# Optimization experiments

Measured on AMD Instinct MI355X. Metric: run time of the kernel, lower is better.

## Reference

```python
import jax, jax.numpy as jnp
import numpy as np

HIDDEN = 768
HEADS = 12
HEAD_DIM = 64
SEQ = 512
DS_K = 64  # downsampling_k
EPS = 1e-6


def setup_inputs() -> dict:
    key = jax.random.key(0)
    ks = jax.random.split(key, 16)
    B = 32
    sd = 1.0 / DS_K
    glorot = jax.nn.initializers.lecun_normal()  # flax default_kernel_init
    inp = {
        "query": jax.random.normal(ks[0], (B, SEQ, HIDDEN), jnp.float32),
        "key": jax.random.normal(ks[1], (B, SEQ, HIDDEN), jnp.float32),
        "value": jax.random.normal(ks[2], (B, SEQ, HIDDEN), jnp.float32),
        "step": 0,
        # learned Linformer-style downsampling projections [k, s]
        "W_kds": sd * jax.random.normal(ks[3], (DS_K, SEQ), jnp.float32),
        "W_vds": sd * jax.random.normal(ks[4], (DS_K, SEQ), jnp.float32),
        # DenseGeneral qkv kernels [d, n, h] and biases [n, h]
        "Wq": glorot(ks[5], (HIDDEN, HEADS, HEAD_DIM), jnp.float32),
        "bq": jnp.zeros((HEADS, HEAD_DIM), jnp.float32),
        "Wk": glorot(ks[6], (HIDDEN, HEADS, HEAD_DIM), jnp.float32),
        "bk": jnp.zeros((HEADS, HEAD_DIM), jnp.float32),
        "Wv": glorot(ks[7], (HIDDEN, HEADS, HEAD_DIM), jnp.float32),
        "bv": jnp.zeros((HEADS, HEAD_DIM), jnp.float32),
        # out projection contracts (n, h) -> hidden
        "Wout": glorot(ks[8], (HEADS * HEAD_DIM, HIDDEN), jnp.float32).reshape(HEADS, HEAD_DIM, HIDDEN),
        "bout": jnp.zeros((HIDDEN,), jnp.float32),
    }
    return inp


def reference(query, key, value, step, W_kds, W_vds, Wq, bq, Wk, bk, Wv, bv, Wout, bout):
    # Linformer-style downsample of keys/values along sequence: [b,s,d] -> [b,k,d]
    key_ds = jnp.einsum("ks,bsd->bkd", W_kds, key)
    val_ds = jnp.einsum("ks,bsd->bkd", W_vds, value)

    # per-head projections
    queries = jnp.einsum("bqd,dnh->bqnh", query, Wq) + bq    # [b,q,n,h]
    keys = jnp.einsum("bkd,dnh->bknh", key_ds, Wk) + bk      # [b,k,n,h]
    values = jnp.einsum("bkd,dnh->bknh", val_ds, Wv) + bv    # [b,k,n,h]

    # kernelized linear attention with elu feature map (mask=False path)
    phi_q = jax.nn.elu(queries) + 1.0
    phi_k = jax.nn.elu(keys) + 1.0
    s = jnp.einsum("bknd,bknh->bndh", phi_k, values)          # [b,n,h,h] KV state
    z = jnp.sum(phi_k, axis=1)                                 # [b,n,h]
    qs = jnp.einsum("bqnd,bndh->bqnh", phi_q, s)
    qz = jnp.einsum("bqnd,bnd->bqn", phi_q, z) + EPS
    a_v = qs / qz[..., None]                                   # [b,q,n,h]

    out = jnp.einsum("bqnh,nhD->bqD", a_v, Wout) + bout        # [b,q,hidden]
    return out
```

## Files before the change

### kernel.cpp

```cpp
#include <hip/hip_runtime.h>

typedef unsigned short u16;
typedef u16 u16x4 __attribute__((ext_vector_type(4)));
typedef u16 u16x8 __attribute__((ext_vector_type(8)));
typedef __bf16 bf16;
typedef bf16 bf16x8 __attribute__((ext_vector_type(8)));
typedef float f32x4 __attribute__((ext_vector_type(4)));

__device__ __forceinline__ float bf2f(u16 v) {
  union { unsigned u; float f; } x; x.u = ((unsigned)v) << 16; return x.f;
}
__device__ __forceinline__ u16 f2bf(float f) {
  union { float f; unsigned u; } x; x.f = f;
  unsigned u = x.u;
  u += 0x7fffu + ((u >> 16) & 1u);
  return (u16)(u >> 16);
}
__device__ __forceinline__ unsigned cvt2bf(float lo, float hi) {
  unsigned r;
  asm("v_cvt_pk_bf16_f32 %0, %1, %2" : "=v"(r) : "v"(lo), "v"(hi));
  return r;
}

#define GLDS16(g, l) __builtin_amdgcn_global_load_lds( \
    (const __attribute__((address_space(1))) unsigned int*)(const void*)(g), \
    (__attribute__((address_space(3))) unsigned int*)(void*)(l), 16, 0, 0)

__global__ __launch_bounds__(256) void prep_k(
    const float* __restrict__ Wq, const float* __restrict__ Wk,
    const float* __restrict__ Wv, const float* __restrict__ Wout,
    const float* __restrict__ wkds, const float* __restrict__ wvds,
    const float* __restrict__ b0, const float* __restrict__ b1,
    const float* __restrict__ b2, const float* __restrict__ b3,
    u16* __restrict__ WT, u16* __restrict__ dstW, u16* __restrict__ dstB)
{
  __shared__ u16 T[64][72];
  const int blk = blockIdx.x;
  const int t = threadIdx.x;
  if (blk < 576) {
    const int bz = blk / 144, rr = blk % 144;
    const int r0 = (rr / 12) * 64, c0 = (rr % 12) * 64;
    const float* W = (bz == 0) ? Wq : (bz == 1) ? Wk : (bz == 2) ? Wv : Wout;
    u16* O = WT + (size_t)bz * 768 * 768;
    #pragma unroll
    for (int p = 0; p < 2; ++p) {
      int v = t + p * 256;
      int r = v / 8, c = (v % 8) * 8;
      f32x4 x0 = *(const f32x4*)&W[(size_t)(r0 + r) * 768 + c0 + c];
      f32x4 x1 = *(const f32x4*)&W[(size_t)(r0 + r) * 768 + c0 + c + 4];
      #pragma unroll
      for (int i = 0; i < 4; ++i) { T[r][c + i] = f2bf(x0[i]); T[r][c + 4 + i] = f2bf(x1[i]); }
    }
    __syncthreads();
    #pragma unroll
    for (int p = 0; p < 2; ++p) {
      int v = t + p * 256;
      int r = v / 8, c = (v % 8) * 8;
      u16x8 tv;
      #pragma unroll
      for (int i = 0; i < 8; ++i) tv[i] = T[c + i][r];
      *(u16x8*)&O[(size_t)(c0 + r) * 768 + r0 + c] = tv;
    }
  } else if (blk < 832) {
    const int i = (blk - 576) * 256 + t;
    if (i < 32768) dstW[i] = f2bf(wkds[i]);
    else           dstW[i] = f2bf(wvds[i - 32768]);
  } else {
    const int i = (blk - 832) * 256 + t;
    if (i < 3072) {
      int s = i / 768, si = i % 768;
      const float* src = (s == 0) ? b0 : (s == 1) ? b1 : (s == 2) ? b2 : b3;
      dstB[i] = f2bf(src[si]);
    }
  }
}

__global__ __launch_bounds__(256) void ds_k(
    const u16* __restrict__ Wds,
    const float* __restrict__ key, const float* __restrict__ value,
    u16* __restrict__ key_ds)
{
  __shared__ u16 Bs[2][64 * 40];
  const int pair = blockIdx.y >> 5, b = blockIdx.y & 31;
  const float* src = (pair ? value : key) + (size_t)b * 512 * 768;
  const u16* W = Wds + pair * 32768;
  u16* dst = key_ds + (size_t)pair * 1572864 + (size_t)b * 49152;
  const int nt = blockIdx.x * 64;
  const int t = threadIdx.x, wave = t >> 6, lane = t & 63;
  const int wm = (wave >> 1) * 32, wn = (wave & 1) * 32;
  const int lrow = lane & 15, quad = lane >> 4;
  const int bn = t & 63, bk8 = (t >> 6) * 8;
  const float* bcol = src + nt + bn;

  f32x4 acc[2][2] = {};
  float breg[8];
  bf16x8 av[2][2];

  #pragma unroll
  for (int i = 0; i < 8; ++i) breg[i] = bcol[(size_t)(bk8 + i) * 768];
  #pragma unroll
  for (int i = 0; i < 2; ++i)
    av[0][i] = *(const bf16x8*)&W[(size_t)(wm + i * 16 + lrow) * 512 + quad * 8];

  #pragma unroll
  for (int step = 0; step < 16; ++step) {
    const int cur = step & 1, nxt = cur ^ 1;
    u16x8 wv;
    #pragma unroll
    for (int i = 0; i < 8; ++i) wv[i] = f2bf(breg[i]);
    *(u16x8*)&Bs[cur][bn * 40 + bk8] = wv;
    if (step < 15) {
      const int k1 = (step + 1) * 32;
      #pragma unroll
      for (int i = 0; i < 8; ++i) breg[i] = bcol[(size_t)(k1 + bk8 + i) * 768];
      #pragma unroll
      for (int i = 0; i < 2; ++i)
        av[nxt][i] = *(const bf16x8*)&W[(size_t)(wm + i * 16 + lrow) * 512 + k1 + quad * 8];
    }
    __syncthreads();
    bf16x8 bv[2];
    #pragma unroll
    for (int j = 0; j < 2; ++j)
      bv[j] = *(const bf16x8*)&Bs[cur][(wn + j * 16 + lrow) * 40 + quad * 8];
    #pragma unroll
    for (int i = 0; i < 2; ++i)
      #pragma unroll
      for (int j = 0; j < 2; ++j)
        acc[i][j] = __builtin_amdgcn_mfma_f32_16x16x32_bf16(av[cur][i], bv[j], acc[i][j], 0, 0, 0);
  }

  #pragma unroll
  for (int i = 0; i < 2; ++i)
    #pragma unroll
    for (int j = 0; j < 2; ++j) {
      const int col = nt + wn + j * 16 + lrow;
      #pragma unroll
      for (int r = 0; r < 4; ++r) {
        const int row = wm + i * 16 + quad * 4 + r;
        dst[(size_t)row * 768 + col] = f2bf(acc[i][j][r]);
      }
    }
}

__global__ __launch_bounds__(256) void gemmqf_k(
    const float* __restrict__ A, const u16* __restrict__ Bt,
    u16* __restrict__ C, const u16* __restrict__ bias)
{
  __shared__ float As[128 * 64];
  __shared__ u16 Bs[128 * 64];
  const int blk = blockIdx.x;
  const int wg = (blk & 7) * 96 + (blk >> 3);
  const int mt = (wg / 6) * 128, nt = (wg % 6) * 128;
  const int t = threadIdx.x, wave = t >> 6, lane = t & 63;
  const int wm = (wave >> 1) * 64, wn = (wave & 1) * 64;
  const int lrow = lane & 15, quad = lane >> 4;
  f32x4 acc[4][4] = {};

  for (int k0 = 0; k0 < 768; k0 += 64) {
    __syncthreads();
    #pragma unroll
    for (int p = 0; p < 8; ++p) {
      const int slot = wave * 512 + p * 64 + lane;
      const int r = slot >> 4, ch = slot & 15;
      const int chs = ch ^ (r & 15);
      GLDS16(&A[(size_t)(mt + r) * 768 + k0 + chs * 4], &As[(wave * 512 + p * 64) * 4]);
    }
    #pragma unroll
    for (int p = 0; p < 4; ++p) {
      const int slot = wave * 256 + p * 64 + lane;
      const int r = slot >> 3, ch = slot & 7;
      const int chs = ch ^ (r & 7);
      GLDS16(&Bt[(size_t)(nt + r) * 768 + k0 + chs * 8], &Bs[(wave * 256 + p * 64) * 8]);
    }
    __syncthreads();

    #pragma unroll
    for (int c = 0; c < 2; ++c) {
      bf16x8 av[4], bv[4];
      #pragma unroll
      for (int i = 0; i < 4; ++i) {
        const int row = wm + i * 16 + lrow;
        const int g0 = c * 8 + 2 * quad;
        f32x4 a0 = *(const f32x4*)&As[row * 64 + ((g0 ^ (row & 15)) * 4)];
        f32x4 a1 = *(const f32x4*)&As[row * 64 + (((g0 + 1) ^ (row & 15)) * 4)];
        union { unsigned w[4]; bf16x8 v; } cv;
        cv.w[0] = cvt2bf(a0[0], a0[1]); cv.w[1] = cvt2bf(a0[2], a0[3]);
        cv.w[2] = cvt2bf(a1[0], a1[1]); cv.w[3] = cvt2bf(a1[2], a1[3]);
        av[i] = cv.v;
      }
      #pragma unroll
      for (int j = 0; j < 4; ++j) {
        const int row = wn + j * 16 + lrow;
        const int g = c * 4 + quad;
        bv[j] = *(const bf16x8*)&Bs[row * 64 + ((g ^ (row & 7)) * 8)];
      }
      #pragma unroll
      for (int i = 0; i < 4; ++i)
        #pragma unroll
        for (int j = 0; j < 4; ++j)
          acc[i][j] = __builtin_amdgcn_mfma_f32_16x16x32_bf16(av[i], bv[j], acc[i][j], 0, 0, 0);
    }
  }

  #pragma unroll
  for (int i = 0; i < 4; ++i) {
    #pragma unroll
    for (int j = 0; j < 4; ++j) {
      const int col = nt + wn + j * 16 + lrow;
      const float badd = bf2f(bias[col]);
      #pragma unroll
      for (int r = 0; r < 4; ++r) {
        const int row = mt + wm + i * 16 + quad * 4 + r;
        float v = acc[i][j][r] + badd;
        v = v > 0.0f ? v + 1.0f : __expf(v);
        C[(size_t)row * 768 + col] = f2bf(v);
      }
    }
  }
}

template<int ACT, bool OF32>
__global__ __launch_bounds__(256) void gemm64_k(
    const u16* __restrict__ A, int lda,
    const u16* __restrict__ Bt, int ldb,
    void* __restrict__ Craw, int ldc,
    const u16* __restrict__ bias, int K)
{
  __shared__ u16 As[128 * 64];
  __shared__ u16 Bs[128 * 64];
  const int blk = blockIdx.x;
  const int wg = (blk & 7) * 96 + (blk >> 3);
  const int mt = (wg / 6) * 128, nt = (wg % 6) * 128;
  const int t = threadIdx.x, wave = t >> 6, lane = t & 63;
  const int wm = (wave >> 1) * 64, wn = (wave & 1) * 64;
  const int lrow = lane & 15, quad = lane >> 4;
  f32x4 acc[4][4] = {};

  for (int k0 = 0; k0 < K; k0 += 64) {
    __syncthreads();
    #pragma unroll
    for (int p = 0; p < 4; ++p) {
      const int slot = wave * 256 + p * 64 + lane;
      const int r = slot >> 3, ch = slot & 7;
      const int chs = ch ^ (r & 7);
      const int lb = (wave * 256 + p * 64) * 8;
      GLDS16(&A[(size_t)(mt + r) * lda + k0 + chs * 8], &As[lb]);
      GLDS16(&Bt[(size_t)(nt + r) * ldb + k0 + chs * 8], &Bs[lb]);
    }
    __syncthreads();

    #pragma unroll
    for (int c = 0; c < 2; ++c) {
      bf16x8 av[4], bv[4];
      #pragma unroll
      for (int i = 0; i < 4; ++i) {
        const int row = wm + i * 16 + lrow;
        const int g = c * 4 + quad;
        av[i] = *(const bf16x8*)&As[row * 64 + ((g ^ (row & 7)) * 8)];
      }
      #pragma unroll
      for (int j = 0; j < 4; ++j) {
        const int row = wn + j * 16 + lrow;
        const int g = c * 4 + quad;
        bv[j] = *(const bf16x8*)&Bs[row * 64 + ((g ^ (row & 7)) * 8)];
      }
      #pragma unroll
      for (int i = 0; i < 4; ++i)
        #pragma unroll
        for (int j = 0; j < 4; ++j)
          acc[i][j] = __builtin_amdgcn_mfma_f32_16x16x32_bf16(av[i], bv[j], acc[i][j], 0, 0, 0);
    }
  }

  #pragma unroll
  for (int i = 0; i < 4; ++i) {
    #pragma unroll
    for (int j = 0; j < 4; ++j) {
      const int col = nt + wn + j * 16 + lrow;
      const float badd = bias ? bf2f(bias[col]) : 0.0f;
      #pragma unroll
      for (int r = 0; r < 4; ++r) {
        const int row = mt + wm + i * 16 + quad * 4 + r;
        float v = acc[i][j][r] + badd;
        if constexpr (ACT == 1) v = v > 0.0f ? v + 1.0f : __expf(v);
        if constexpr (OF32) ((float*)Craw)[(size_t)row * ldc + col] = v;
        else                ((u16*)Craw)[(size_t)row * ldc + col] = f2bf(v);
      }
    }
  }
}

__global__ __launch_bounds__(256) void fkv_k(
    const u16* __restrict__ key_ds,
    const u16* __restrict__ WT,
    const u16* __restrict__ bias_c,
    u16* __restrict__ sT, float* __restrict__ z)
{
  __shared__ char sm[32768];
  u16* T0 = (u16*)sm;
  u16* Pt = (u16*)sm;
  u16* Vt = (u16*)(sm + 9216);
  const int x = blockIdx.x;
  const int b = x / 12, n = x % 12;
  const int t = threadIdx.x, wave = t >> 6, lane = t & 63;
  const u16* srcs[4] = {
    key_ds + (size_t)b * 49152,
    WT + 589824 + (size_t)n * 49152,
    key_ds + 1572864 + (size_t)b * 49152,
    WT + 2 * 589824 + (size_t)n * 49152 };
  const int grow = lane >> 3;
  const int gchunk = (lane & 7) ^ (grow & 7);
  const int isV = wave & 1;
  const int wm = (wave >> 1) * 32;
  u16* Atile = T0 + (isV ? 2 : 0) * 4096;
  u16* Btile = T0 + (isV ? 3 : 1) * 4096;
  const int lrow = lane & 15, quad = lane >> 4;
  f32x4 acc[2][4] = {};

  for (int k0 = 0; k0 < 768; k0 += 64) {
    const u16* s = srcs[wave];
    u16* dtile = T0 + wave * 4096;
    #pragma unroll
    for (int j = 0; j < 8; ++j) {
      const u16* gsrc = s + (size_t)(j * 8 + grow) * 768 + k0 + gchunk * 8;
      GLDS16(gsrc, (char*)dtile + j * 1024);
    }
    __syncthreads();
    #pragma unroll
    for (int c = 0; c < 2; ++c) {
      bf16x8 av[2], bv[4];
      #pragma unroll
      for (int i = 0; i < 2; ++i) {
        const int row = wm + i * 16 + lrow;
        av[i] = *(const bf16x8*)&Atile[row * 64 + (((c * 4 + quad) ^ (row & 7)) * 8)];
      }
      #pragma unroll
      for (int j = 0; j < 4; ++j) {
        const int row = j * 16 + lrow;
        bv[j] = *(const bf16x8*)&Btile[row * 64 + (((c * 4 + quad) ^ (row & 7)) * 8)];
      }
      #pragma unroll
      for (int i = 0; i < 2; ++i)
        #pragma unroll
        for (int j = 0; j < 4; ++j)
          acc[i][j] = __builtin_amdgcn_mfma_f32_16x16x32_bf16(av[i], bv[j], acc[i][j], 0, 0, 0);
    }
    __syncthreads();
  }

  const u16* bias = bias_c + (isV ? 1536 : 768) + n * 64;
  u16* Ttile = isV ? Vt : Pt;
  #pragma unroll
  for (int i = 0; i < 2; ++i)
    #pragma unroll
    for (int j = 0; j < 4; ++j) {
      const int col = j * 16 + lrow;
      const float badd = bf2f(bias[col]);
      u16x4 pk4;
      #pragma unroll
      for (int r = 0; r < 4; ++r) {
        float v = acc[i][j][r] + badd;
        if (!isV) v = v > 0.0f ? v + 1.0f : __expf(v);
        pk4[r] = f2bf(v);
      }
      *(u16x4*)&Ttile[col * 72 + wm + i * 16 + quad * 4] = pk4;
    }
  __syncthreads();

  const int wm2 = (wave >> 1) * 32, wn2 = (wave & 1) * 32;
  f32x4 a2[2][2] = {};
  #pragma unroll
  for (int c = 0; c < 2; ++c) {
    bf16x8 av[2], bv[2];
    #pragma unroll
    for (int i = 0; i < 2; ++i)
      av[i] = *(const bf16x8*)&Vt[(wm2 + i * 16 + lrow) * 72 + c * 32 + quad * 8];
    #pragma unroll
    for (int j = 0; j < 2; ++j)
      bv[j] = *(const bf16x8*)&Pt[(wn2 + j * 16 + lrow) * 72 + c * 32 + quad * 8];
    #pragma unroll
    for (int i = 0; i < 2; ++i)
      #pragma unroll
      for (int j = 0; j < 2; ++j)
        a2[i][j] = __builtin_amdgcn_mfma_f32_16x16x32_bf16(av[i], bv[j], a2[i][j], 0, 0, 0);
  }
  u16* sTg = sT + (size_t)x * 4096;
  #pragma unroll
  for (int i = 0; i < 2; ++i)
    #pragma unroll
    for (int j = 0; j < 2; ++j)
      #pragma unroll
      for (int r = 0; r < 4; ++r)
        sTg[(size_t)(wm2 + i * 16 + quad * 4 + r) * 64 + wn2 + j * 16 + lrow] = f2bf(a2[i][j][r]);
  if (t < 64) {
    float zz = 0.f;
    #pragma unroll
    for (int g = 0; g < 8; ++g) {
      u16x8 p = *(const u16x8*)&Pt[t * 72 + g * 8];
      #pragma unroll
      for (int e = 0; e < 8; ++e) zz += bf2f(p[e]);
    }
    z[(size_t)x * 64 + t] = zz;
  }
}

__global__ __launch_bounds__(256) void attn_av_k(
    u16* __restrict__ phi_q, const u16* __restrict__ sT, const float* __restrict__ zbuf)
{
  __shared__ u16 As[64 * 72];
  __shared__ u16 Bs[64 * 72];
  __shared__ float zv[64];
  __shared__ float zpart[4][64];
  __shared__ float zq[64];
  const int x = blockIdx.x, y = blockIdx.y;
  const int b = y / 12, n = y % 12;
  const int t = threadIdx.x;
  u16* Abase = phi_q + (size_t)b * 512 * 768 + (size_t)x * 64 * 768 + n * 64;
  const u16* Bbase = sT + (size_t)y * 4096;
  if (t < 64) zv[t] = zbuf[(size_t)y * 64 + t];
  #pragma unroll
  for (int p = 0; p < 2; ++p) {
    int v = t + p * 256;
    int r = v >> 3, c = (v & 7) * 8;
    *(u16x8*)&As[r * 72 + c] = *(const u16x8*)&Abase[(size_t)r * 768 + c];
    *(u16x8*)&Bs[r * 72 + c] = *(const u16x8*)&Bbase[r * 64 + c];
  }
  __syncthreads();
  {
    int r = t & 63, seg = t >> 6;
    float s = 0.f;
    #pragma unroll
    for (int j = 0; j < 16; ++j) s += bf2f(As[r * 72 + seg * 16 + j]) * zv[seg * 16 + j];
    zpart[seg][r] = s;
  }
  __syncthreads();
  if (t < 64) {
    float s = zpart[0][t] + zpart[1][t] + zpart[2][t] + zpart[3][t];
    zq[t] = 1.0f / (s + 1e-6f);
  }
  const int wave = t >> 6, lane = t & 63;
  const int wm = (wave >> 1) * 32, wn = (wave & 1) * 32;
  const int lrow = lane & 15, quad = lane >> 4;
  f32x4 acc[2][2] = {};
  #pragma unroll
  for (int c = 0; c < 2; ++c) {
    bf16x8 av[2], bv[2];
    #pragma unroll
    for (int i = 0; i < 2; ++i) av[i] = *(const bf16x8*)&As[(wm + i * 16 + lrow) * 72 + c * 32 + quad * 8];
    #pragma unroll
    for (int j = 0; j < 2; ++j) bv[j] = *(const bf16x8*)&Bs[(wn + j * 16 + lrow) * 72 + c * 32 + quad * 8];
    #pragma unroll
    for (int i = 0; i < 2; ++i)
      #pragma unroll
      for (int j = 0; j < 2; ++j)
        acc[i][j] = __builtin_amdgcn_mfma_f32_16x16x32_bf16(av[i], bv[j], acc[i][j], 0, 0, 0);
  }
  __syncthreads();
  #pragma unroll
  for (int i = 0; i < 2; ++i)
    #pragma unroll
    for (int j = 0; j < 2; ++j) {
      const int col = wn + j * 16 + lrow;
      #pragma unroll
      for (int r = 0; r < 4; ++r) {
        const int row = wm + i * 16 + quad * 4 + r;
        Abase[(size_t)row * 768 + col] = f2bf(acc[i][j][r] * zq[row]);
      }
    }
}

__global__ void tagfill_k(float* out, float val, int n) {
  int i = blockIdx.x * 256 + threadIdx.x;
  if (i < n) out[i] = val;
}

extern "C" void kernel_launch(void* const* d_in, const int* in_sizes, int n_in,
                              void* d_out, int out_size, void* d_ws, size_t ws_size,
                              hipStream_t stream) {
  (void)out_size;
  float* out = (float*)d_out;

  int o;
  if (n_in >= 14 && in_sizes[3] == 1) o = 4;
  else if (n_in == 13) o = 3;
  else { tagfill_k<<<4, 256, 0, stream>>>(out, 77.0f, 1024); return; }
  if (in_sizes[0] != 12582912 || in_sizes[o + 0] != 32768 || in_sizes[o + 2] != 589824) {
    tagfill_k<<<4, 256, 0, stream>>>(out, 88.0f, 1024); return;
  }

  const float* query = (const float*)d_in[0];
  const float* key   = (const float*)d_in[1];
  const float* value = (const float*)d_in[2];
  const float* W_kds = (const float*)d_in[o + 0];
  const float* W_vds = (const float*)d_in[o + 1];
  const float* Wq   = (const float*)d_in[o + 2];
  const float* bq   = (const float*)d_in[o + 3];
  const float* Wk   = (const float*)d_in[o + 4];
  const float* bk   = (const float*)d_in[o + 5];
  const float* Wv   = (const float*)d_in[o + 6];
  const float* bv   = (const float*)d_in[o + 7];
  const float* Wout = (const float*)d_in[o + 8];
  const float* bout = (const float*)d_in[o + 9];

  const size_t NEED = 61478912;
  if (ws_size < NEED) { tagfill_k<<<4, 256, 0, stream>>>(out, 123.0f, 1024); return; }

  char* base = (char*)d_ws;
  u16*   WT     = (u16*)base;
  char*  Breg   = base + 4718592;
  u16*   sT     = (u16*)Breg;
  float* zbuf   = (float*)(Breg + 3145728);
  u16*   phi_q  = (u16*)(base + 29884416);
  u16*   bias_c = (u16*)(base + 55181312);
  u16*   key_ds = (u16*)(base + 55187456);
  u16*   Wds_c  = (u16*)(base + 55050240);
  u16* a_v = phi_q;
  u16* WqT   = WT;
  u16* WoutT = WT + 3 * 768 * 768;
  u16* bq_c = bias_c, *bout_c = bias_c + 2304;

  prep_k<<<844, 256, 0, stream>>>(Wq, Wk, Wv, Wout, W_kds, W_vds,
                                  bq, bk, bv, bout, WT, Wds_c, bias_c);

  gemmqf_k<<<768, 256, 0, stream>>>(query, WqT, phi_q, bq_c);

  ds_k<<<dim3(12, 64), 256, 0, stream>>>(Wds_c, key, value, key_ds);

  fkv_k<<<384, 256, 0, stream>>>(key_ds, WT, bias_c, sT, zbuf);

  attn_av_k<<<dim3(8, 384), 256, 0, stream>>>(phi_q, sT, zbuf);

  gemm64_k<0, true><<<768, 256, 0, stream>>>(
      a_v, 768, WoutT, 768, out, 768, bout_c, 768);
}
```

Before: 297.7 us.

## Fuse attention apply into output projection and pre-convert query to bf16

```diff
diff --git a/kernel.cpp b/kernel.cpp
--- a/kernel.cpp
+++ b/kernel.cpp
@@ -16,10 +16,10 @@
   u += 0x7fffu + ((u >> 16) & 1u);
   return (u16)(u >> 16);
 }
-__device__ __forceinline__ unsigned cvt2bf(float lo, float hi) {
-  unsigned r;
-  asm("v_cvt_pk_bf16_f32 %0, %1, %2" : "=v"(r) : "v"(lo), "v"(hi));
-  return r;
+
+__device__ __forceinline__ void bar_lgkm() {
+  asm volatile("s_waitcnt lgkmcnt(0)" ::: "memory");
+  __builtin_amdgcn_s_barrier();
 }
 
 #define GLDS16(g, l) __builtin_amdgcn_global_load_lds( \
@@ -29,10 +29,12 @@
 __global__ __launch_bounds__(256) void prep_k(
     const float* __restrict__ Wq, const float* __restrict__ Wk,
     const float* __restrict__ Wv, const float* __restrict__ Wout,
+    const float* __restrict__ query,
     const float* __restrict__ wkds, const float* __restrict__ wvds,
     const float* __restrict__ b0, const float* __restrict__ b1,
     const float* __restrict__ b2, const float* __restrict__ b3,
-    u16* __restrict__ WT, u16* __restrict__ dstW, u16* __restrict__ dstB)
+    u16* __restrict__ WT, u16* __restrict__ q_bf,
+    u16* __restrict__ dstW, u16* __restrict__ dstB)
 {
   __shared__ u16 T[64][72];
   const int blk = blockIdx.x;
@@ -61,16 +63,22 @@
       for (int i = 0; i < 8; ++i) tv[i] = T[c + i][r];
       *(u16x8*)&O[(size_t)(c0 + r) * 768 + r0 + c] = tv;
     }
-  } else if (blk < 832) {
-    const int i = (blk - 576) * 256 + t;
-    if (i < 32768) dstW[i] = f2bf(wkds[i]);
-    else           dstW[i] = f2bf(wvds[i - 32768]);
+  } else if (blk < 6720) {
+    const size_t i = (size_t)(blk - 576) * 256 + t;
+    f32x4 a = *(const f32x4*)&query[i * 8];
+    f32x4 b = *(const f32x4*)&query[i * 8 + 4];
+    u16x8 w;
+    #pragma unroll
+    for (int j = 0; j < 4; ++j) { w[j] = f2bf(a[j]); w[4 + j] = f2bf(b[j]); }
+    *(u16x8*)&q_bf[i * 8] = w;
   } else {
-    const int i = (blk - 832) * 256 + t;
-    if (i < 3072) {
-      int s = i / 768, si = i % 768;
+    const int i = (blk - 6720) * 256 + t;
+    if (i < 32768)      dstW[i] = f2bf(wkds[i]);
+    else if (i < 65536) dstW[i] = f2bf(wvds[i - 32768]);
+    else {
+      int j = i - 65536, s = j / 768, si = j % 768;
       const float* src = (s == 0) ? b0 : (s == 1) ? b1 : (s == 2) ? b2 : b3;
-      dstB[i] = f2bf(src[si]);
+      dstB[j] = f2bf(src[si]);
     }
   }
 }
@@ -117,7 +125,7 @@
       for (int i = 0; i < 2; ++i)
         av[nxt][i] = *(const bf16x8*)&W[(size_t)(wm + i * 16 + lrow) * 512 + k1 + quad * 8];
     }
-    __syncthreads();
+    bar_lgkm();
     bf16x8 bv[2];
     #pragma unroll
     for (int j = 0; j < 2; ++j)
@@ -140,83 +148,6 @@
         dst[(size_t)row * 768 + col] = f2bf(acc[i][j][r]);
       }
     }
-}
-
-__global__ __launch_bounds__(256) void gemmqf_k(
-    const float* __restrict__ A, const u16* __restrict__ Bt,
-    u16* __restrict__ C, const u16* __restrict__ bias)
-{
-  __shared__ float As[128 * 64];
-  __shared__ u16 Bs[128 * 64];
-  const int blk = blockIdx.x;
-  const int wg = (blk & 7) * 96 + (blk >> 3);
-  const int mt = (wg / 6) * 128, nt = (wg % 6) * 128;
-  const int t = threadIdx.x, wave = t >> 6, lane = t & 63;
-  const int wm = (wave >> 1) * 64, wn = (wave & 1) * 64;
-  const int lrow = lane & 15, quad = lane >> 4;
-  f32x4 acc[4][4] = {};
-
-  for (int k0 = 0; k0 < 768; k0 += 64) {
-    __syncthreads();
-    #pragma unroll
-    for (int p = 0; p < 8; ++p) {
-      const int slot = wave * 512 + p * 64 + lane;
-      const int r = slot >> 4, ch = slot & 15;
-      const int chs = ch ^ (r & 15);
-      GLDS16(&A[(size_t)(mt + r) * 768 + k0 + chs * 4], &As[(wave * 512 + p * 64) * 4]);
-    }
-    #pragma unroll
-    for (int p = 0; p < 4; ++p) {
-      const int slot = wave * 256 + p * 64 + lane;
-      const int r = slot >> 3, ch = slot & 7;
-      const int chs = ch ^ (r & 7);
-      GLDS16(&Bt[(size_t)(nt + r) * 768 + k0 + chs * 8], &Bs[(wave * 256 + p * 64) * 8]);
-    }
-    __syncthreads();
-
-    #pragma unroll
-    for (int c = 0; c < 2; ++c) {
-      bf16x8 av[4], bv[4];
-      #pragma unroll
-      for (int i = 0; i < 4; ++i) {
-        const int row = wm + i * 16 + lrow;
-        const int g0 = c * 8 + 2 * quad;
-        f32x4 a0 = *(const f32x4*)&As[row * 64 + ((g0 ^ (row & 15)) * 4)];
-        f32x4 a1 = *(const f32x4*)&As[row * 64 + (((g0 + 1) ^ (row & 15)) * 4)];
-        union { unsigned w[4]; bf16x8 v; } cv;
-        cv.w[0] = cvt2bf(a0[0], a0[1]); cv.w[1] = cvt2bf(a0[2], a0[3]);
-        cv.w[2] = cvt2bf(a1[0], a1[1]); cv.w[3] = cvt2bf(a1[2], a1[3]);
-        av[i] = cv.v;
-      }
-      #pragma unroll
-      for (int j = 0; j < 4; ++j) {
-        const int row = wn + j * 16 + lrow;
-        const int g = c * 4 + quad;
-        bv[j] = *(const bf16x8*)&Bs[row * 64 + ((g ^ (row & 7)) * 8)];
-      }
-      #pragma unroll
-      for (int i = 0; i < 4; ++i)
-        #pragma unroll
-        for (int j = 0; j < 4; ++j)
-          acc[i][j] = __builtin_amdgcn_mfma_f32_16x16x32_bf16(av[i], bv[j], acc[i][j], 0, 0, 0);
-    }
-  }
-
-  #pragma unroll
-  for (int i = 0; i < 4; ++i) {
-    #pragma unroll
-    for (int j = 0; j < 4; ++j) {
-      const int col = nt + wn + j * 16 + lrow;
-      const float badd = bf2f(bias[col]);
-      #pragma unroll
-      for (int r = 0; r < 4; ++r) {
-        const int row = mt + wm + i * 16 + quad * 4 + r;
-        float v = acc[i][j][r] + badd;
-        v = v > 0.0f ? v + 1.0f : __expf(v);
-        C[(size_t)row * 768 + col] = f2bf(v);
-      }
-    }
-  }
 }
 
 template<int ACT, bool OF32>
@@ -255,14 +186,12 @@
       #pragma unroll
       for (int i = 0; i < 4; ++i) {
         const int row = wm + i * 16 + lrow;
-        const int g = c * 4 + quad;
-        av[i] = *(const bf16x8*)&As[row * 64 + ((g ^ (row & 7)) * 8)];
+        av[i] = *(const bf16x8*)&As[row * 64 + (((c * 4 + quad) ^ (row & 7)) * 8)];
       }
       #pragma unroll
       for (int j = 0; j < 4; ++j) {
         const int row = wn + j * 16 + lrow;
-        const int g = c * 4 + quad;
-        bv[j] = *(const bf16x8*)&Bs[row * 64 + ((g ^ (row & 7)) * 8)];
+        bv[j] = *(const bf16x8*)&Bs[row * 64 + (((c * 4 + quad) ^ (row & 7)) * 8)];
       }
       #pragma unroll
       for (int i = 0; i < 4; ++i)
@@ -404,69 +333,134 @@
   }
 }
 
-__global__ __launch_bounds__(256) void attn_av_k(
-    u16* __restrict__ phi_q, const u16* __restrict__ sT, const float* __restrict__ zbuf)
+__global__ __launch_bounds__(256) void gemmav_k(
+    const u16* __restrict__ phi_q,
+    const u16* __restrict__ sT,
+    const float* __restrict__ zbuf,
+    const u16* __restrict__ WoutT,
+    float* __restrict__ out, const u16* __restrict__ bias)
 {
-  __shared__ u16 As[64 * 72];
-  __shared__ u16 Bs[64 * 72];
-  __shared__ float zv[64];
-  __shared__ float zpart[4][64];
-  __shared__ float zq[64];
-  const int x = blockIdx.x, y = blockIdx.y;
-  const int b = y / 12, n = y % 12;
-  const int t = threadIdx.x;
-  u16* Abase = phi_q + (size_t)b * 512 * 768 + (size_t)x * 64 * 768 + n * 64;
-  const u16* Bbase = sT + (size_t)y * 4096;
-  if (t < 64) zv[t] = zbuf[(size_t)y * 64 + t];
-  #pragma unroll
-  for (int p = 0; p < 2; ++p) {
-    int v = t + p * 256;
-    int r = v >> 3, c = (v & 7) * 8;
-    *(u16x8*)&As[r * 72 + c] = *(const u16x8*)&Abase[(size_t)r * 768 + c];
-    *(u16x8*)&Bs[r * 72 + c] = *(const u16x8*)&Bbase[r * 64 + c];
-  }
-  __syncthreads();
-  {
-    int r = t & 63, seg = t >> 6;
-    float s = 0.f;
-    #pragma unroll
-    for (int j = 0; j < 16; ++j) s += bf2f(As[r * 72 + seg * 16 + j]) * zv[seg * 16 + j];
-    zpart[seg][r] = s;
-  }
-  __syncthreads();
-  if (t < 64) {
-    float s = zpart[0][t] + zpart[1][t] + zpart[2][t] + zpart[3][t];
-    zq[t] = 1.0f / (s + 1e-6f);
-  }
-  const int wave = t >> 6, lane = t & 63;
-  const int wm = (wave >> 1) * 32, wn = (wave & 1) * 32;
+  __shared__ u16 PA[128 * 72];
+  __shared__ u16 Sv[64 * 64];
+  __shared__ u16 Bs[128 * 64];
+  __shared__ float zl[64];
+  __shared__ float zp[2][128];
+  __shared__ float zq[128];
+  const int blk = blockIdx.x;
+  const int wg = (blk & 7) * 96 + (blk >> 3);
+  const int mt = (wg / 6) * 128, nt = (wg % 6) * 128;
+  const int xb = (mt >> 9) * 12;
+  const int t = threadIdx.x, wave = t >> 6, lane = t & 63;
+  const int wm = (wave >> 1) * 64, wn = (wave & 1) * 64;
   const int lrow = lane & 15, quad = lane >> 4;
-  f32x4 acc[2][2] = {};
-  #pragma unroll
-  for (int c = 0; c < 2; ++c) {
-    bf16x8 av[2], bv[2];
-    #pragma unroll
-    for (int i = 0; i < 2; ++i) av[i] = *(const bf16x8*)&As[(wm + i * 16 + lrow) * 72 + c * 32 + quad * 8];
-    #pragma unroll
-    for (int j = 0; j < 2; ++j) bv[j] = *(const bf16x8*)&Bs[(wn + j * 16 + lrow) * 72 + c * 32 + quad * 8];
-    #pragma unroll
-    for (int i = 0; i < 2; ++i)
-      #pragma unroll
-      for (int j = 0; j < 2; ++j)
-        acc[i][j] = __builtin_amdgcn_mfma_f32_16x16x32_bf16(av[i], bv[j], acc[i][j], 0, 0, 0);
-  }
-  __syncthreads();
-  #pragma unroll
-  for (int i = 0; i < 2; ++i)
-    #pragma unroll
-    for (int j = 0; j < 2; ++j) {
-      const int col = wn + j * 16 + lrow;
+  const int wi = wave * 32;
+  const int zr = t >> 1, zh = t & 1;
+  f32x4 acc[4][4] = {};
+
+  for (int h = 0; h < 12; ++h) {
+    if (t < 64) zl[t] = zbuf[(size_t)(xb + h) * 64 + t];
+    const u16* pqs = phi_q + (size_t)mt * 768 + h * 64;
+    const u16* svs = sT + (size_t)(xb + h) * 4096;
+    const u16* bts = WoutT + (size_t)nt * 768 + h * 64;
+    #pragma unroll
+    for (int p = 0; p < 4; ++p) {
+      const int slot = wave * 256 + p * 64 + lane;
+      const int r = slot >> 3, ch = slot & 7;
+      const int chs = ch ^ (r & 7);
+      GLDS16(&pqs[(size_t)r * 768 + chs * 8], &PA[(wave * 256 + p * 64) * 8]);
+      GLDS16(&bts[(size_t)r * 768 + chs * 8], &Bs[(wave * 256 + p * 64) * 8]);
+    }
+    #pragma unroll
+    for (int p = 0; p < 2; ++p) {
+      const int slot = wave * 128 + p * 64 + lane;
+      const int r = slot >> 3, ch = slot & 7;
+      const int chs = ch ^ (r & 7);
+      GLDS16(&svs[r * 64 + chs * 8], &Sv[(wave * 128 + p * 64) * 8]);
+    }
+    __syncthreads();
+
+    {
+      float s = 0.f;
+      #pragma unroll
+      for (int dc = 0; dc < 4; ++dc) {
+        const int ch = zh * 4 + dc;
+        u16x8 pv = *(const u16x8*)&PA[zr * 64 + ((ch ^ (zr & 7)) * 8)];
+        #pragma unroll
+        for (int e = 0; e < 8; ++e) s += bf2f(pv[e]) * zl[ch * 8 + e];
+      }
+      zp[zh][zr] = s;
+    }
+    __syncthreads();
+    if (t < 128) zq[t] = 1.0f / (zp[0][t] + zp[1][t] + 1e-6f);
+
+    f32x4 a1[2][4] = {};
+    #pragma unroll
+    for (int c = 0; c < 2; ++c) {
+      bf16x8 av[2], bv[4];
+      #pragma unroll
+      for (int i2 = 0; i2 < 2; ++i2) {
+        const int row = wi + i2 * 16 + lrow;
+        av[i2] = *(const bf16x8*)&PA[row * 64 + (((c * 4 + quad) ^ (row & 7)) * 8)];
+      }
+      #pragma unroll
+      for (int j = 0; j < 4; ++j) {
+        const int rw = j * 16 + lrow;
+        bv[j] = *(const bf16x8*)&Sv[rw * 64 + (((c * 4 + quad) ^ (rw & 7)) * 8)];
+      }
+      #pragma unroll
+      for (int i2 = 0; i2 < 2; ++i2)
+        #pragma unroll
+        for (int j = 0; j < 4; ++j)
+          a1[i2][j] = __builtin_amdgcn_mfma_f32_16x16x32_bf16(av[i2], bv[j], a1[i2][j], 0, 0, 0);
+    }
+    __syncthreads();
+
+    #pragma unroll
+    for (int i2 = 0; i2 < 2; ++i2)
+      #pragma unroll
+      for (int j = 0; j < 4; ++j) {
+        const int col = j * 16 + lrow;
+        #pragma unroll
+        for (int r = 0; r < 4; ++r) {
+          const int row = wi + i2 * 16 + quad * 4 + r;
+          PA[row * 72 + col] = f2bf(a1[i2][j][r] * zq[row]);
+        }
+      }
+    __syncthreads();
+
+    #pragma unroll
+    for (int c = 0; c < 2; ++c) {
+      bf16x8 av2[4], bv2[4];
+      #pragma unroll
+      for (int i = 0; i < 4; ++i)
+        av2[i] = *(const bf16x8*)&PA[(wm + i * 16 + lrow) * 72 + (c * 4 + quad) * 8];
+      #pragma unroll
+      for (int j = 0; j < 4; ++j) {
+        const int rw = wn + j * 16 + lrow;
+        bv2[j] = *(const bf16x8*)&Bs[rw * 64 + (((c * 4 + quad) ^ (rw & 7)) * 8)];
+      }
+      #pragma unroll
+      for (int i = 0; i < 4; ++i)
+        #pragma unroll
+        for (int j = 0; j < 4; ++j)
+          acc[i][j] = __builtin_amdgcn_mfma_f32_16x16x32_bf16(av2[i], bv2[j], acc[i][j], 0, 0, 0);
+    }
+    __syncthreads();
+  }
+
+  #pragma unroll
+  for (int i = 0; i < 4; ++i) {
+    #pragma unroll
+    for (int j = 0; j < 4; ++j) {
+      const int col = nt + wn + j * 16 + lrow;
+      const float badd = bf2f(bias[col]);
       #pragma unroll
       for (int r = 0; r < 4; ++r) {
-        const int row = wm + i * 16 + quad * 4 + r;
-        Abase[(size_t)row * 768 + col] = f2bf(acc[i][j][r] * zq[row]);
-      }
-    }
+        const int row = mt + wm + i * 16 + quad * 4 + r;
+        out[(size_t)row * 768 + col] = acc[i][j][r] + badd;
+      }
+    }
+  }
 }
 
 __global__ void tagfill_k(float* out, float val, int n) {
@@ -508,28 +502,26 @@
   char* base = (char*)d_ws;
   u16*   WT     = (u16*)base;
   char*  Breg   = base + 4718592;
+  u16*   q_bf   = (u16*)Breg;
   u16*   sT     = (u16*)Breg;
   float* zbuf   = (float*)(Breg + 3145728);
   u16*   phi_q  = (u16*)(base + 29884416);
+  u16*   Wds_c  = (u16*)(base + 55050240);
   u16*   bias_c = (u16*)(base + 55181312);
   u16*   key_ds = (u16*)(base + 55187456);
-  u16*   Wds_c  = (u16*)(base + 55050240);
-  u16* a_v = phi_q;
   u16* WqT   = WT;
   u16* WoutT = WT + 3 * 768 * 768;
   u16* bq_c = bias_c, *bout_c = bias_c + 2304;
 
-  prep_k<<<844, 256, 0, stream>>>(Wq, Wk, Wv, Wout, W_kds, W_vds,
-                                  bq, bk, bv, bout, WT, Wds_c, bias_c);
-
-  gemmqf_k<<<768, 256, 0, stream>>>(query, WqT, phi_q, bq_c);
+  prep_k<<<6988, 256, 0, stream>>>(Wq, Wk, Wv, Wout, query, W_kds, W_vds,
+                                   bq, bk, bv, bout, WT, q_bf, Wds_c, bias_c);
+
+  gemm64_k<1, false><<<768, 256, 0, stream>>>(
+      q_bf, 768, WqT, 768, phi_q, 768, bq_c, 768);
 
   ds_k<<<dim3(12, 64), 256, 0, stream>>>(Wds_c, key, value, key_ds);
 
   fkv_k<<<384, 256, 0, stream>>>(key_ds, WT, bias_c, sT, zbuf);
 
-  attn_av_k<<<dim3(8, 384), 256, 0, stream>>>(phi_q, sT, zbuf);
-
-  gemm64_k<0, true><<<768, 256, 0, stream>>>(
-      a_v, 768, WoutT, 768, out, 768, bout_c, 768);
-}
+  gemmav_k<<<768, 256, 0, stream>>>(phi_q, sT, zbuf, WoutT, out, bout_c);
+}
```

New measurement: 311.2 us. 4.5% more time.
